# Kernel optimization log

Measured on AMD Instinct MI355X. Metric: run time of the kernel, lower is better.

The kernel has to match this reference:

```python
import jax, jax.numpy as jnp
import numpy as np
import math

B = 1024      # graphs
N = 64        # nodes per graph (padded, masked by node_mask)
BN = B * N    # total nodes
EPG = 192     # directed edges per graph
E = B * EPG


def setup_inputs() -> dict:
    key = jax.random.key(0)
    ks = jax.random.split(key, 40)

    def nrm(k, shp, s=0.02):
        return (jax.random.normal(k, shp) * s).astype(jnp.float32)

    mol_batch_x = jax.random.normal(ks[0], (BN, 19), dtype=jnp.float32)
    offs = jnp.arange(B, dtype=jnp.int32) * N
    src = jax.random.randint(ks[1], (B, EPG), 0, N, dtype=jnp.int32) + offs[:, None]
    dst = jax.random.randint(ks[2], (B, EPG), 0, N, dtype=jnp.int32) + offs[:, None]
    mol_batch_edge_index = jnp.stack([src.reshape(-1), dst.reshape(-1)], axis=0)
    mol_batch_batch = jnp.repeat(jnp.arange(B, dtype=jnp.int32), N)
    text_features = jax.random.normal(ks[3], (B, 300), dtype=jnp.float32)
    timesteps = jax.random.uniform(ks[4], (B,), minval=0.0, maxval=1000.0, dtype=jnp.float32)
    node_mask = (jax.random.uniform(ks[5], (B, N)) > 0.1).astype(jnp.float32)

    p = {
        'W_tr': nrm(ks[6], (19, 300)),   'b_tr': jnp.zeros((300,), jnp.float32),
        'W_c1': nrm(ks[7], (300, 600)),  'b_c1': jnp.zeros((600,), jnp.float32),
        'W_c2': nrm(ks[8], (600, 600)),  'b_c2': jnp.zeros((600,), jnp.float32),
        'W_c3': nrm(ks[9], (600, 600)),  'b_c3': jnp.zeros((600,), jnp.float32),
        'W_h1': nrm(ks[10], (600, 600)), 'b_h1': jnp.zeros((600,), jnp.float32),
        'W_h2': nrm(ks[11], (600, 600)), 'b_h2': jnp.zeros((600,), jnp.float32),
        'W_h3': nrm(ks[12], (600, 300)), 'b_h3': jnp.zeros((300,), jnp.float32),
        'ln_g': jnp.ones((300,), jnp.float32), 'ln_b': jnp.zeros((300,), jnp.float32),
        'W_t1': nrm(ks[13], (128, 512)), 'b_t1': jnp.zeros((512,), jnp.float32),
        'W_t2': nrm(ks[14], (512, 512)), 'b_t2': jnp.zeros((512,), jnp.float32),
        'W_e':  nrm(ks[15], (512, 3000)), 'b_e': jnp.zeros((3000,), jnp.float32),
    }
    return dict(mol_batch_x=mol_batch_x, mol_batch_edge_index=mol_batch_edge_index,
                mol_batch_batch=mol_batch_batch, text_features=text_features,
                timesteps=timesteps, node_mask=node_mask, **p)


def timestep_embedding(t, dim=128, max_period=10000.0):
    half = dim // 2
    freqs = jnp.exp(-math.log(max_period) * jnp.arange(half, dtype=jnp.float32) / half)
    args = t[:, None] * freqs[None]                 # [B, half]
    return jnp.concatenate([jnp.cos(args), jnp.sin(args)], axis=-1)  # [B, dim]


def gcn_conv(x, W, b, src, dst, num_nodes):
    # PyG GCNConv: D^{-1/2} (A + I) D^{-1/2} X W + b, edge weights 1
    h = x @ W                                             # [BN, F]
    deg = jnp.zeros((num_nodes,), h.dtype).at[dst].add(1.0) + 1.0  # in-degree + self-loop
    inv_sqrt = jax.lax.rsqrt(deg)
    coef = inv_sqrt[src] * inv_sqrt[dst]                  # [E]
    agg = jax.ops.segment_sum(h[src] * coef[:, None], dst, num_segments=num_nodes)
    return agg + h * (1.0 / deg)[:, None] + b             # self-loop norm = 1/deg


def global_mean_pool(x, batch, num_graphs):
    sums = jax.ops.segment_sum(x, batch, num_segments=num_graphs)
    cnts = jax.ops.segment_sum(jnp.ones((x.shape[0],), x.dtype), batch, num_segments=num_graphs)
    return sums / jnp.maximum(cnts, 1.0)[:, None]


def layer_norm(x, g, b, eps=1e-5):
    mu = jnp.mean(x, axis=-1, keepdims=True)
    var = jnp.mean(jnp.square(x - mu), axis=-1, keepdims=True)
    return (x - mu) * jax.lax.rsqrt(var + eps) * g + b


def reference(mol_batch_x, mol_batch_edge_index, mol_batch_batch, text_features,
              timesteps, node_mask, W_tr, b_tr, W_c1, b_c1, W_c2, b_c2, W_c3, b_c3,
              W_h1, b_h1, W_h2, b_h2, W_h3, b_h3, ln_g, ln_b,
              W_t1, b_t1, W_t2, b_t2, W_e, b_e):
    num_nodes = mol_batch_x.shape[0]
    num_graphs = node_mask.shape[0]
    src, dst = mol_batch_edge_index[0], mol_batch_edge_index[1]

    # FiLM conditioning from timestep embedding
    emb = jax.nn.relu(timestep_embedding(timesteps, 128) @ W_t1 + b_t1) @ W_t2 + b_t2  # [B,512]
    emb_out = jax.nn.relu(emb) @ W_e + b_e                                             # [B,3000]
    s1, t1 = emb_out[:, 0:600], emb_out[:, 600:1200]
    s2, t2 = emb_out[:, 1200:1800], emb_out[:, 1800:2400]
    s3, t3 = emb_out[:, 2400:2700], emb_out[:, 2700:3000]

    # node transform + mask
    x = mol_batch_x @ W_tr + b_tr                     # [BN, 300]
    x = x * node_mask.reshape(-1, 1)

    # GCN stack
    x = jax.nn.relu(gcn_conv(x, W_c1, b_c1, src, dst, num_nodes))
    x = jax.nn.relu(gcn_conv(x, W_c2, b_c2, src, dst, num_nodes))
    x = gcn_conv(x, W_c3, b_c3, src, dst, num_nodes)  # [BN, 600]

    g = global_mean_pool(x, mol_batch_batch, num_graphs)  # [B, 600]
    g = jax.nn.relu(g @ W_h1 + b_h1)
    g = g * (1.0 + s1) + t1
    g = jax.nn.relu(g @ W_h2 + b_h2)
    g = g * (1.0 + s2) + t2
    g = g @ W_h3 + b_h3                                # [B, 300]
    g = g * (1.0 + s3) + t3
    g = layer_norm(g, ln_g, ln_b)
    return (g, text_features)
```

## Files before the change

kernel.cpp:

```cpp
#include <hip/hip_runtime.h>
#include <hip/hip_bf16.h>
#include <cstdint>
#include <cstddef>

static constexpr int B   = 1024;
static constexpr int N   = 64;
static constexpr int BN  = B * N;
static constexpr int EPG = 192;
static constexpr int E   = B * EPG;
static constexpr int FP  = 608;
static constexpr int PMS = 80;
static constexpr int NCONV = 2560;

typedef __hip_bfloat16 bf16;
typedef __bf16 bf16x8 __attribute__((ext_vector_type(8)));
typedef __bf16 bf16x4 __attribute__((ext_vector_type(4)));
typedef float  f32x4  __attribute__((ext_vector_type(4)));

__device__ __forceinline__ void storeC(float* p, float v) { *p = v; }
__device__ __forceinline__ void storeC(bf16* p, float v) { *p = __float2bfloat16(v); }

__device__ __forceinline__ void llds16(const void* g, void* l) {
    __builtin_amdgcn_global_load_lds(
        (const __attribute__((address_space(1))) unsigned int*)g,
        (__attribute__((address_space(3))) unsigned int*)l,
        16, 0, 0);
}

template<bool RELU, bool FILM, typename CT>
__device__ __forceinline__ void g64_tile(
    const bf16* __restrict__ A, int lda,
    const bf16* __restrict__ Bt, int ldb,
    const float* __restrict__ bias,
    CT* __restrict__ C, int ldc, int Ncap,
    const bf16* __restrict__ fS, const bf16* __restrict__ fT, int fstride,
    int K, int m0, int n0, __bf16* As, __bf16* Bs, int tid)
{
    const int lane = tid & 63;
    const int w    = tid >> 6;
    const int wn   = w * 32;
    const int l15  = lane & 15;
    const int lhi  = lane >> 4;

    f32x4 acc[4][2] = {};

    for (int k0 = 0; k0 < K; k0 += 32) {
        {
            int row = tid >> 2, kc = tid & 3;
            char* la = (char*)As + (size_t)(w * 64) * 16;
            llds16(A + (size_t)(m0 + row) * lda + k0 + kc * 8, la);
        }
        #pragma unroll
        for (int t = 0; t < 2; ++t) {
            int ci  = t * 256 + tid;
            int row = ci >> 2, kc = ci & 3;
            char* lb = (char*)Bs + (size_t)(t * 256 + w * 64) * 16;
            llds16(Bt + (size_t)(n0 + row) * ldb + k0 + kc * 8, lb);
        }
        asm volatile("s_waitcnt vmcnt(0)" ::: "memory");
        __syncthreads();

        bf16x8 af[4], bg[2];
        #pragma unroll
        for (int i = 0; i < 4; ++i)
            af[i] = *(bf16x8*)(As + (i * 16 + l15) * 32 + lhi * 8);
        #pragma unroll
        for (int j = 0; j < 2; ++j)
            bg[j] = *(bf16x8*)(Bs + (wn + j * 16 + l15) * 32 + lhi * 8);
        #pragma unroll
        for (int i = 0; i < 4; ++i)
            #pragma unroll
            for (int j = 0; j < 2; ++j)
                acc[i][j] = __builtin_amdgcn_mfma_f32_16x16x32_bf16(
                    af[i], bg[j], acc[i][j], 0, 0, 0);
        __syncthreads();
    }

    #pragma unroll
    for (int i = 0; i < 4; ++i) {
        #pragma unroll
        for (int j = 0; j < 2; ++j) {
            int col = n0 + wn + j * 16 + l15;
            if (col < Ncap) {
                float bv = bias ? bias[col] : 0.f;
                #pragma unroll
                for (int e = 0; e < 4; ++e) {
                    int row = m0 + i * 16 + lhi * 4 + e;
                    float v = acc[i][j][e] + bv;
                    if (RELU) v = fmaxf(v, 0.f);
                    if (FILM) {
                        float sv = __bfloat162float(fS[(size_t)row * fstride + col]);
                        float tv = __bfloat162float(fT[(size_t)row * fstride + col]);
                        v = v * (1.f + sv) + tv;
                    }
                    storeC(&C[(size_t)row * ldc + col], v);
                }
            }
        }
    }
}

template<bool RELU, bool FILM, typename CT>
__global__ __launch_bounds__(256) void gemm64(
    const bf16* __restrict__ A, int lda,
    const bf16* __restrict__ Bt, int ldb,
    const float* __restrict__ bias,
    CT* __restrict__ C, int ldc, int Ncap,
    const bf16* __restrict__ fS, const bf16* __restrict__ fT, int fstride,
    int K)
{
    __shared__ __align__(16) __bf16 As[64 * 32];
    __shared__ __align__(16) __bf16 Bs[128 * 32];
    g64_tile<RELU, FILM, CT>(A, lda, Bt, ldb, bias, C, ldc, Ncap,
                             fS, fT, fstride, K,
                             blockIdx.x * 64, blockIdx.y * 128, As, Bs,
                             threadIdx.x);
}

__global__ __launch_bounds__(256) void k_two_gemms(
    const bf16* __restrict__ A2b, const bf16* __restrict__ Wet,
    const float* __restrict__ b_e, bf16* __restrict__ EO,
    const bf16* __restrict__ Yv, const bf16* __restrict__ Wb3,
    const float* __restrict__ b_c3, bf16* __restrict__ G0)
{
    __shared__ __align__(16) __bf16 As[64 * 32];
    __shared__ __align__(16) __bf16 Bs[128 * 32];
    int bid = blockIdx.x;
    if (bid < 384) {
        int mt = bid / 24, nt = bid % 24;
        g64_tile<false, false, bf16>(A2b, 512, Wet, 512, b_e, EO, 3000, 3000,
                                     nullptr, nullptr, 0, 512,
                                     mt * 64, nt * 128, As, Bs, threadIdx.x);
    } else {
        int t = bid - 384;
        int mt = t / 5, nt = t % 5;
        g64_tile<false, false, bf16>(Yv, FP, Wb3, FP, b_c3, G0, FP, 600,
                                     nullptr, nullptr, 0, FP,
                                     mt * 64, nt * 128, As, Bs, threadIdx.x);
    }
}

__global__ __launch_bounds__(256) void conv_fused(
    const bf16* __restrict__ A, int lda, int K,
    const bf16* __restrict__ Bt, int ldb,
    const bf16* __restrict__ Pmg,
    const float* __restrict__ bias,
    bf16* __restrict__ Xout,
    const bf16* __restrict__ gA, int glda,
    const bf16* __restrict__ gBt, int gldb,
    const float* __restrict__ gbias,
    bf16* __restrict__ gC, int gldc, int gNcap, int gK, int gnt)
{
    __shared__ __align__(16) char regA[17408];
    __shared__ __align__(16) __bf16 Pm[128 * PMS];

    const int tid = threadIdx.x;
    const int bid = blockIdx.x;

    if (bid >= NCONV) {
        int t = bid - NCONV;
        int mt2 = t / gnt, nt2 = t % gnt;
        g64_tile<true, false, bf16>(gA, glda, gBt, gldb, gbias, gC, gldc, gNcap,
                                    nullptr, nullptr, 0, gK,
                                    mt2 * 64, nt2 * 128,
                                    (__bf16*)regA, (__bf16*)(regA + 4096), tid);
        return;
    }

    __bf16* As = (__bf16*)regA;
    __bf16* Bs = (__bf16*)(regA + 8192);
    __bf16* Ts = (__bf16*)regA;

    const int lane = tid & 63;
    const int w    = tid >> 6;
    const int wm   = (w & 1) * 64;
    const int wn   = (w >> 1) * 64;
    const int l15  = lane & 15;
    const int lhi  = lane >> 4;

    const int lid = bid >> 3;
    const int mt  = (bid & 7) * 64 + lid / 5;
    const int nt  = lid % 5;
    const int m0  = mt * 128;
    const int n0  = nt * 128;

    #pragma unroll
    for (int i = 0; i < 5; ++i) {
        int cbase = w * 320 + i * 64;
        llds16(Pmg + (size_t)mt * (128 * PMS) + (size_t)(cbase + lane) * 8,
               (char*)Pm + (size_t)cbase * 16);
    }

    f32x4 acc[4][4] = {};
    for (int k0 = 0; k0 < K; k0 += 32) {
        #pragma unroll
        for (int t = 0; t < 2; ++t) {
            int ci  = t * 256 + w * 64 + lane;
            int row = ci >> 2, kc = ci & 3;
            char* la = (char*)As + (size_t)(t * 256 + w * 64) * 16;
            char* lb = (char*)Bs + (size_t)(t * 256 + w * 64) * 16;
            llds16(A  + (size_t)(m0 + row) * lda + k0 + kc * 8, la);
            llds16(Bt + (size_t)(n0 + row) * ldb + k0 + kc * 8, lb);
        }
        asm volatile("s_waitcnt vmcnt(0)" ::: "memory");
        __syncthreads();

        bf16x8 af[4], bg[4];
        #pragma unroll
        for (int i = 0; i < 4; ++i)
            af[i] = *(bf16x8*)(As + (wm + i * 16 + l15) * 32 + lhi * 8);
        #pragma unroll
        for (int j = 0; j < 4; ++j)
            bg[j] = *(bf16x8*)(Bs + (wn + j * 16 + l15) * 32 + lhi * 8);
        #pragma unroll
        for (int i = 0; i < 4; ++i)
            #pragma unroll
            for (int j = 0; j < 4; ++j)
                acc[i][j] = __builtin_amdgcn_mfma_f32_16x16x32_bf16(
                    af[i], bg[j], acc[i][j], 0, 0, 0);
        __syncthreads();
    }

    const int g  = w & 1;
    const int nb = w >> 1;
    #pragma unroll
    for (int h = 0; h < 2; ++h) {
        if (wn == h * 64) {
            #pragma unroll
            for (int i = 0; i < 4; ++i)
                #pragma unroll
                for (int j = 0; j < 4; ++j) {
                    int c_local = j * 16 + l15;
                    int rbase   = wm + i * 16 + lhi * 4;
                    bf16x4 pk;
                    #pragma unroll
                    for (int e = 0; e < 4; ++e) pk[e] = (__bf16)acc[i][j][e];
                    *(bf16x4*)(Ts + c_local * 136 + rbase) = pk;
                }
        }
        __syncthreads();

        f32x4 acc2[4][2] = {};
        #pragma unroll
        for (int k0 = 0; k0 < 64; k0 += 32) {
            bf16x8 pa[4], hb[2];
            #pragma unroll
            for (int i = 0; i < 4; ++i)
                pa[i] = *(bf16x8*)(Pm + (g * 64 + i * 16 + l15) * PMS + k0 + lhi * 8);
            #pragma unroll
            for (int j = 0; j < 2; ++j)
                hb[j] = *(bf16x8*)(Ts + (nb * 32 + j * 16 + l15) * 136
                                      + g * 64 + k0 + lhi * 8);
            #pragma unroll
            for (int i = 0; i < 4; ++i)
                #pragma unroll
                for (int j = 0; j < 2; ++j)
                    acc2[i][j] = __builtin_amdgcn_mfma_f32_16x16x32_bf16(
                        pa[i], hb[j], acc2[i][j], 0, 0, 0);
        }
        #pragma unroll
        for (int i = 0; i < 4; ++i)
            #pragma unroll
            for (int j = 0; j < 2; ++j) {
                int col = n0 + h * 64 + nb * 32 + j * 16 + l15;
                if (col < FP) {
                    float bv = (col < 600) ? bias[col] : 0.f;
                    #pragma unroll
                    for (int e = 0; e < 4; ++e) {
                        int row = m0 + g * 64 + i * 16 + lhi * 4 + e;
                        float v = fmaxf(acc2[i][j][e] + bv, 0.f);
                        Xout[(size_t)row * FP + col] = __float2bfloat16(v);
                    }
                }
            }
        __syncthreads();
    }
}

__global__ __launch_bounds__(256) void conv_fused_q(
    const bf16* __restrict__ A, int lda, int K,
    const bf16* __restrict__ Bt, int ldb,
    const bf16* __restrict__ Pmg,
    const float* __restrict__ bias,
    const float* __restrict__ qv,
    bf16* __restrict__ Y,
    const bf16* __restrict__ gA, int glda,
    const bf16* __restrict__ gBt, int gldb,
    const float* __restrict__ gbias,
    bf16* __restrict__ gC, int gldc, int gNcap, int gK, int gnt)
{
    __shared__ __align__(16) char regA[17408];
    __shared__ __align__(16) __bf16 Pm[128 * PMS];
    __shared__ float s_q[128];

    const int tid = threadIdx.x;
    const int bid = blockIdx.x;

    if (bid >= NCONV) {
        int t = bid - NCONV;
        int mt2 = t / gnt, nt2 = t % gnt;
        g64_tile<true, false, bf16>(gA, glda, gBt, gldb, gbias, gC, gldc, gNcap,
                                    nullptr, nullptr, 0, gK,
                                    mt2 * 64, nt2 * 128,
                                    (__bf16*)regA, (__bf16*)(regA + 4096), tid);
        return;
    }

    __bf16* As = (__bf16*)regA;
    __bf16* Bs = (__bf16*)(regA + 8192);
    __bf16* Ts = (__bf16*)regA;

    const int lane = tid & 63;
    const int w    = tid >> 6;
    const int wm   = (w & 1) * 64;
    const int wn   = (w >> 1) * 64;
    const int l15  = lane & 15;
    const int lhi  = lane >> 4;

    const int lid = bid >> 3;
    const int mt  = (bid & 7) * 64 + lid / 5;
    const int nt  = lid % 5;
    const int m0  = mt * 128;
    const int n0  = nt * 128;

    #pragma unroll
    for (int i = 0; i < 5; ++i) {
        int cbase = w * 320 + i * 64;
        llds16(Pmg + (size_t)mt * (128 * PMS) + (size_t)(cbase + lane) * 8,
               (char*)Pm + (size_t)cbase * 16);
    }
    if (tid < 128) s_q[tid] = qv[mt * 128 + tid];

    f32x4 acc[4][4] = {};
    for (int k0 = 0; k0 < K; k0 += 32) {
        #pragma unroll
        for (int t = 0; t < 2; ++t) {
            int ci  = t * 256 + w * 64 + lane;
            int row = ci >> 2, kc = ci & 3;
            char* la = (char*)As + (size_t)(t * 256 + w * 64) * 16;
            char* lb = (char*)Bs + (size_t)(t * 256 + w * 64) * 16;
            llds16(A  + (size_t)(m0 + row) * lda + k0 + kc * 8, la);
            llds16(Bt + (size_t)(n0 + row) * ldb + k0 + kc * 8, lb);
        }
        asm volatile("s_waitcnt vmcnt(0)" ::: "memory");
        __syncthreads();

        bf16x8 af[4], bg[4];
        #pragma unroll
        for (int i = 0; i < 4; ++i)
            af[i] = *(bf16x8*)(As + (wm + i * 16 + l15) * 32 + lhi * 8);
        #pragma unroll
        for (int j = 0; j < 4; ++j)
            bg[j] = *(bf16x8*)(Bs + (wn + j * 16 + l15) * 32 + lhi * 8);
        #pragma unroll
        for (int i = 0; i < 4; ++i)
            #pragma unroll
            for (int j = 0; j < 4; ++j)
                acc[i][j] = __builtin_amdgcn_mfma_f32_16x16x32_bf16(
                    af[i], bg[j], acc[i][j], 0, 0, 0);
        __syncthreads();
    }

    const int g  = w & 1;
    const int nb = w >> 1;
    #pragma unroll
    for (int h = 0; h < 2; ++h) {
        if (wn == h * 64) {
            #pragma unroll
            for (int i = 0; i < 4; ++i)
                #pragma unroll
                for (int j = 0; j < 4; ++j) {
                    int c_local = j * 16 + l15;
                    int rbase   = wm + i * 16 + lhi * 4;
                    bf16x4 pk;
                    #pragma unroll
                    for (int e = 0; e < 4; ++e) pk[e] = (__bf16)acc[i][j][e];
                    *(bf16x4*)(Ts + c_local * 136 + rbase) = pk;
                }
        }
        __syncthreads();

        f32x4 acc2[4][2] = {};
        #pragma unroll
        for (int k0 = 0; k0 < 64; k0 += 32) {
            bf16x8 pa[4], hb[2];
            #pragma unroll
            for (int i = 0; i < 4; ++i)
                pa[i] = *(bf16x8*)(Pm + (g * 64 + i * 16 + l15) * PMS + k0 + lhi * 8);
            #pragma unroll
            for (int j = 0; j < 2; ++j)
                hb[j] = *(bf16x8*)(Ts + (nb * 32 + j * 16 + l15) * 136
                                      + g * 64 + k0 + lhi * 8);
            #pragma unroll
            for (int i = 0; i < 4; ++i)
                #pragma unroll
                for (int j = 0; j < 2; ++j)
                    acc2[i][j] = __builtin_amdgcn_mfma_f32_16x16x32_bf16(
                        pa[i], hb[j], acc2[i][j], 0, 0, 0);
        }
        #pragma unroll
        for (int j = 0; j < 2; ++j) {
            int col = n0 + h * 64 + nb * 32 + j * 16 + l15;
            float bv = (col < 600) ? bias[col] : 0.f;
            float yp = 0.f;
            #pragma unroll
            for (int i = 0; i < 4; ++i)
                #pragma unroll
                for (int e = 0; e < 4; ++e) {
                    float v = fmaxf(acc2[i][j][e] + bv, 0.f);
                    yp += s_q[g * 64 + i * 16 + lhi * 4 + e] * v;
                }
            yp += __shfl_xor(yp, 16, 64);
            yp += __shfl_xor(yp, 32, 64);
            if (lhi == 0 && col < FP)
                Y[(size_t)(mt * 2 + g) * FP + col] = __float2bfloat16(yp);
        }
        __syncthreads();
    }
}

struct WtJob  { const float* src; bf16* dst; int Ksrc, Nsrc, Kp, Np, blk0; };
struct PrepArgs {
    WtJob j[9];
    int nwt, te0, pp0, xtr0;
    const int*   ei;
    const float* ts;
    const float* xin; const float* Wtr; const float* btr; const float* mask;
    bf16* TE; bf16* Pmg; float* qv; bf16* X;
};

__global__ __launch_bounds__(256) void k_prep(PrepArgs a)
{
    __shared__ __align__(16) char sm[35840];
    const int bx  = blockIdx.x;
    const int tid = threadIdx.x;

    if (bx < a.nwt) {
        int ji = 0;
        while (ji < 8 && bx >= a.j[ji + 1].blk0) ++ji;
        WtJob jb = a.j[ji];
        int t  = bx - jb.blk0;
        int kt = (jb.Kp + 63) >> 6;
        int ti = t % kt, tj = t / kt;
        int kg0 = ti * 64, ng0 = tj * 64;
        float (*T)[65] = (float(*)[65])sm;
        #pragma unroll 4
        for (int r = 0; r < 16; ++r) {
            int kl = (tid >> 6) + r * 4, nl = tid & 63;
            int kg = kg0 + kl, ng = ng0 + nl;
            T[kl][nl] = (kg < jb.Ksrc && ng < jb.Nsrc)
                        ? jb.src[(size_t)kg * jb.Nsrc + ng] : 0.f;
        }
        __syncthreads();
        #pragma unroll 4
        for (int r = 0; r < 16; ++r) {
            int nl = (tid >> 6) + r * 4, kl = tid & 63;
            int ng = ng0 + nl, kg = kg0 + kl;
            if (ng < jb.Np && kg < jb.Kp)
                jb.dst[(size_t)ng * jb.Kp + kg] = __float2bfloat16(T[kl][nl]);
        }
    } else if (bx < a.pp0) {
        int idx = (bx - a.te0) * 256 + tid;
        int b = idx >> 7, jj = idx & 127;
        float tt = a.ts[b];
        int h = jj & 63;
        float freq = expf(-9.210340371976184f * (float)h / 64.f);
        float ang = tt * freq;
        a.TE[idx] = __float2bfloat16((jj < 64) ? cosf(ang) : sinf(ang));
    } else if (bx < a.xtr0) {
        int pr = bx - a.pp0;
        float* Pf   = (float*)sm;
        int*   cnt  = (int*)(sm + 32768);
        float* sQ   = (float*)(sm + 33280);
        float* sI   = (float*)(sm + 33792);
        float* sIvd = (float*)(sm + 34304);

        for (int idx = tid; idx < 8192; idx += 256) Pf[idx] = 0.f;
        if (tid < 128) cnt[tid] = 0;
        __syncthreads();
        for (int e = tid; e < 2 * EPG; e += 256) {
            int g  = (e >= EPG);
            int eg = (2 * pr + g) * EPG + (e - g * EPG);
            int ld = (a.ei[E + eg] & 63) + g * 64;
            atomicAdd(&cnt[ld], 1);
        }
        __syncthreads();
        if (tid < 128) {
            float d = (float)cnt[tid] + 1.0f;
            float iv = 1.f / d;
            sIvd[tid] = iv;
            sI[tid]   = rsqrtf(d);
            sQ[tid]   = iv;
        }
        __syncthreads();
        for (int e = tid; e < 2 * EPG; e += 256) {
            int g   = (e >= EPG);
            int eg  = (2 * pr + g) * EPG + (e - g * EPG);
            int lsl = a.ei[eg] & 63;
            int ldl = a.ei[E + eg] & 63;
            float cf = sI[g * 64 + lsl] * sI[g * 64 + ldl];
            atomicAdd(&Pf[(g * 64 + ldl) * 64 + lsl], cf);
            atomicAdd(&sQ[g * 64 + lsl], cf);
        }
        __syncthreads();
        if (tid < 128) {
            Pf[tid * 64 + (tid & 63)] += sIvd[tid];
            a.qv[pr * 128 + tid] = sQ[tid] * (1.f / 64.f);
        }
        __syncthreads();
        for (int idx = tid; idx < 128 * PMS; idx += 256) {
            int r = idx / PMS, k = idx - r * PMS;
            float v = (k < 64) ? Pf[r * 64 + k] : 0.f;
            a.Pmg[(size_t)pr * (128 * PMS) + idx] = __float2bfloat16(v);
        }
    } else {
        int g = bx - a.xtr0;
        float* Ws = (float*)sm;
        float* xb = (float*)(sm + 23104);
        float* sb = (float*)(sm + 28224);
        float* smk= (float*)(sm + 29440);

        for (int idx = tid; idx < 19 * 304; idx += 256) {
            int k = idx / 304, c = idx - k * 304;
            Ws[idx] = (c < 300) ? a.Wtr[k * 300 + c] : 0.f;
        }
        for (int idx = tid; idx < 64 * 19; idx += 256) {
            int n = idx / 19, k = idx - n * 19;
            xb[n * 20 + k] = a.xin[(size_t)(g * 64 + n) * 19 + k];
        }
        for (int c = tid; c < 304; c += 256)
            sb[c] = (c < 300) ? a.btr[c] : 0.f;
        if (tid < 64) smk[tid] = a.mask[g * 64 + tid];
        __syncthreads();

        int n  = tid >> 2;
        int c0 = tid & 3;
        float m = smk[n];
        for (int c = c0; c < 304; c += 4) {
            float acc = sb[c];
            #pragma unroll
            for (int k = 0; k < 19; ++k)
                acc += xb[n * 20 + k] * Ws[k * 304 + c];
            a.X[(size_t)(g * 64 + n) * FP + c] = __float2bfloat16(acc * m);
        }
        bf16x8 z = {};
        for (int idx = tid; idx < 64 * 38; idx += 256) {
            int nn = idx / 38, jv = idx - nn * 38;
            *(bf16x8*)((__bf16*)a.X + (size_t)(g * 64 + nn) * FP + 304 + jv * 8) = z;
        }
    }
}

__global__ __launch_bounds__(256) void k_ln_copy(const float* __restrict__ G,
                                                 const float* __restrict__ lg,
                                                 const float* __restrict__ lb,
                                                 const float* __restrict__ text,
                                                 float* __restrict__ out)
{
    int r = blockIdx.x;
    int tid = threadIdx.x;
    __shared__ float red[4];
    __shared__ float smu, svar;

    float v0 = (tid < 300) ? G[r * 300 + tid] : 0.f;
    float v1 = (tid + 256 < 300) ? G[r * 300 + tid + 256] : 0.f;
    float s = v0 + v1;
    #pragma unroll
    for (int o = 32; o > 0; o >>= 1) s += __shfl_down(s, o, 64);
    if ((tid & 63) == 0) red[tid >> 6] = s;
    __syncthreads();
    if (tid == 0) smu = (red[0] + red[1] + red[2] + red[3]) * (1.f / 300.f);
    __syncthreads();
    float mu = smu;
    float d0 = (tid < 300) ? v0 - mu : 0.f;
    float d1 = (tid + 256 < 300) ? v1 - mu : 0.f;
    s = d0 * d0 + d1 * d1;
    #pragma unroll
    for (int o = 32; o > 0; o >>= 1) s += __shfl_down(s, o, 64);
    if ((tid & 63) == 0) red[tid >> 6] = s;
    __syncthreads();
    if (tid == 0) svar = (red[0] + red[1] + red[2] + red[3]) * (1.f / 300.f);
    __syncthreads();
    float rstd = rsqrtf(svar + 1e-5f);
    if (tid < 300)
        out[r * 300 + tid] = d0 * rstd * lg[tid] + lb[tid];
    if (tid + 256 < 300)
        out[r * 300 + tid + 256] = d1 * rstd * lg[tid + 256] + lb[tid + 256];
    float* o2 = out + (size_t)B * 300;
    for (int c = tid; c < 300; c += 256)
        o2[(size_t)r * 300 + c] = text[(size_t)r * 300 + c];
}

extern "C" void kernel_launch(void* const* d_in, const int* in_sizes, int n_in,
                              void* d_out, int out_size, void* d_ws, size_t ws_size,
                              hipStream_t stream)
{
    const float* x_in  = (const float*)d_in[0];
    const int*   ei    = (const int*)d_in[1];
    const float* text  = (const float*)d_in[3];
    const float* tst   = (const float*)d_in[4];
    const float* mask  = (const float*)d_in[5];
    const float* W_tr  = (const float*)d_in[6];
    const float* b_tr  = (const float*)d_in[7];
    const float* W_c1  = (const float*)d_in[8];
    const float* b_c1  = (const float*)d_in[9];
    const float* W_c2  = (const float*)d_in[10];
    const float* b_c2  = (const float*)d_in[11];
    const float* W_c3  = (const float*)d_in[12];
    const float* b_c3  = (const float*)d_in[13];
    const float* W_h1  = (const float*)d_in[14];
    const float* b_h1  = (const float*)d_in[15];
    const float* W_h2  = (const float*)d_in[16];
    const float* b_h2  = (const float*)d_in[17];
    const float* W_h3  = (const float*)d_in[18];
    const float* b_h3  = (const float*)d_in[19];
    const float* ln_g  = (const float*)d_in[20];
    const float* ln_b  = (const float*)d_in[21];
    const float* W_t1  = (const float*)d_in[22];
    const float* b_t1  = (const float*)d_in[23];
    const float* W_t2  = (const float*)d_in[24];
    const float* b_t2  = (const float*)d_in[25];
    const float* W_e   = (const float*)d_in[26];
    const float* b_e   = (const float*)d_in[27];

    char* w = (char*)d_ws;
    size_t off = 0;
    auto carve = [&](size_t bytes) {
        void* p = w + off;
        off += (bytes + 255) & ~(size_t)255;
        return p;
    };
    bf16*  XA     = (bf16*) carve((size_t)BN * FP * 2);
    bf16*  Wb1    = (bf16*) carve((size_t)640 * 320 * 2);
    bf16*  Wb2    = (bf16*) carve((size_t)640 * FP * 2);
    bf16*  Wb3    = (bf16*) carve((size_t)640 * FP * 2);
    bf16*  Wt1t   = (bf16*) carve((size_t)512 * 128 * 2);
    bf16*  Wt2t   = (bf16*) carve((size_t)512 * 512 * 2);
    bf16*  Wet    = (bf16*) carve((size_t)3072 * 512 * 2);
    bf16*  Wh1t   = (bf16*) carve((size_t)640 * FP * 2);
    bf16*  Wh2t   = (bf16*) carve((size_t)640 * FP * 2);
    bf16*  Wh3t   = (bf16*) carve((size_t)384 * FP * 2);
    bf16*  TE     = (bf16*) carve((size_t)B * 128 * 2);
    bf16*  A1b    = (bf16*) carve((size_t)B * 512 * 2);
    bf16*  A2b    = (bf16*) carve((size_t)B * 512 * 2);
    bf16*  EO     = (bf16*) carve((size_t)B * 3000 * 2);
    bf16*  Yv     = (bf16*) carve((size_t)B * FP * 2);
    bf16*  G0     = (bf16*) carve((size_t)B * FP * 2);
    bf16*  G1     = (bf16*) carve((size_t)B * FP * 2);
    bf16*  G2     = (bf16*) carve((size_t)B * FP * 2);
    float* G3     = (float*)carve((size_t)B * 300 * 4);
    bf16*  Pmg    = (bf16*) carve((size_t)512 * 128 * PMS * 2);
    float* qv     = (float*)carve((size_t)BN * 4);
    (void)ws_size; (void)in_sizes; (void)n_in; (void)out_size;

    float* out = (float*)d_out;

    PrepArgs pa;
    struct JD { const float* s; bf16* d; int Ks, Ns, Kp, Np; };
    JD jd[9] = {
        { W_c1, Wb1,  300, 600,  320, 640 },
        { W_c2, Wb2,  600, 600,  FP,  640 },
        { W_c3, Wb3,  600, 600,  FP,  640 },
        { W_t1, Wt1t, 128, 512,  128, 512 },
        { W_t2, Wt2t, 512, 512,  512, 512 },
        { W_e,  Wet,  512, 3000, 512, 3072 },
        { W_h1, Wh1t, 600, 600,  FP,  640 },
        { W_h2, Wh2t, 600, 600,  FP,  640 },
        { W_h3, Wh3t, 600, 300,  FP,  384 },
    };
    int cum = 0;
    for (int i = 0; i < 9; ++i) {
        int kt = (jd[i].Kp + 63) >> 6, nt = (jd[i].Np + 63) >> 6;
        pa.j[i] = { jd[i].s, jd[i].d, jd[i].Ks, jd[i].Ns, jd[i].Kp, jd[i].Np, cum };
        cum += kt * nt;
    }
    pa.nwt  = cum;
    pa.te0  = cum;       cum += (B * 128) / 256;
    pa.pp0  = cum;       cum += B / 2;
    pa.xtr0 = cum;       cum += B;
    pa.ei = ei; pa.ts = tst;
    pa.xin = x_in; pa.Wtr = W_tr; pa.btr = b_tr; pa.mask = mask;
    pa.TE = TE; pa.Pmg = Pmg; pa.qv = qv; pa.X = XA;
    k_prep<<<cum, 256, 0, stream>>>(pa);

    conv_fused<<<NCONV + 64, 256, 0, stream>>>(
        XA, FP, 320, Wb1, 320, Pmg, b_c1, XA,
        TE, 128, Wt1t, 128, b_t1, A1b, 512, 512, 128, 4);

    conv_fused_q<<<NCONV + 64, 256, 0, stream>>>(
        XA, FP, FP, Wb2, FP, Pmg, b_c2, qv, Yv,
        A1b, 512, Wt2t, 512, b_t2, A2b, 512, 512, 512, 4);

    k_two_gemms<<<464, 256, 0, stream>>>(A2b, Wet, b_e, EO, Yv, Wb3, b_c3, G0);

    gemm64<true, true, bf16><<<dim3(16, 5), 256, 0, stream>>>(
        G0, FP, Wh1t, FP, b_h1, G1, FP, 600, EO + 0, EO + 600, 3000, FP);
    gemm64<true, true, bf16><<<dim3(16, 5), 256, 0, stream>>>(
        G1, FP, Wh2t, FP, b_h2, G2, FP, 600, EO + 1200, EO + 1800, 3000, FP);
    gemm64<false, true, float><<<dim3(16, 3), 256, 0, stream>>>(
        G2, FP, Wh3t, FP, b_h3, G3, 300, 300, EO + 2400, EO + 2700, 3000, FP);

    k_ln_copy<<<B, 256, 0, stream>>>(G3, ln_g, ln_b, text, out);
}
```

Before: 408.0 us.

## Aggregate first GCN layer on 20-wide inputs before the node transform

The first conv layer's normalized adjacency is now applied in k_prep to the masked 19-feature input (plus a mask column for the bias), using the associativity P(XW+b) = (PX)W + (P·mask)b. The first conv kernel then becomes a plain GEMM with ReLU, with no per-tile P·H MFMA pass and no Pm LDS staging. This removes the second matmul stage and its extra LDS traffic and syncs from the large conv1 launch, but adds per-graph shared-memory atomics and a small dense 64x64x20 product to the prep kernel. The guest GEMM path is also moved into a noinline helper, which may reduce register pressure in the main kernels.

```diff
diff --git a/kernel.cpp b/kernel.cpp
--- a/kernel.cpp
+++ b/kernel.cpp
@@ -9,6 +9,7 @@
 static constexpr int EPG = 192;
 static constexpr int E   = B * EPG;
 static constexpr int FP  = 608;
+static constexpr int KP1 = 320;
 static constexpr int PMS = 80;
 static constexpr int NCONV = 2560;
 
@@ -100,6 +101,17 @@
     }
 }
 
+__device__ __attribute__((noinline)) void guest_g64(
+    const bf16* gA, int glda, const bf16* gBt, int gldb,
+    const float* gbias, bf16* gC, int gldc, int gNcap, int gK, int gnt,
+    int t, char* lds, int tid)
+{
+    int mt2 = t / gnt, nt2 = t % gnt;
+    g64_tile<true, false, bf16>(gA, glda, gBt, gldb, gbias, gC, gldc, gNcap,
+                                nullptr, nullptr, 0, gK, mt2 * 64, nt2 * 128,
+                                (__bf16*)lds, (__bf16*)(lds + 4096), tid);
+}
+
 template<bool RELU, bool FILM, typename CT>
 __global__ __launch_bounds__(256) void gemm64(
     const bf16* __restrict__ A, int lda,
@@ -140,36 +152,28 @@
     }
 }
 
-__global__ __launch_bounds__(256) void conv_fused(
-    const bf16* __restrict__ A, int lda, int K,
-    const bf16* __restrict__ Bt, int ldb,
-    const bf16* __restrict__ Pmg,
+__global__ __launch_bounds__(256) void conv1_gemm(
+    const bf16* __restrict__ A,
+    const bf16* __restrict__ Bt,
     const float* __restrict__ bias,
-    bf16* __restrict__ Xout,
+    bf16* __restrict__ X1,
     const bf16* __restrict__ gA, int glda,
     const bf16* __restrict__ gBt, int gldb,
     const float* __restrict__ gbias,
     bf16* __restrict__ gC, int gldc, int gNcap, int gK, int gnt)
 {
     __shared__ __align__(16) char regA[17408];
-    __shared__ __align__(16) __bf16 Pm[128 * PMS];
-
     const int tid = threadIdx.x;
     const int bid = blockIdx.x;
 
     if (bid >= NCONV) {
-        int t = bid - NCONV;
-        int mt2 = t / gnt, nt2 = t % gnt;
-        g64_tile<true, false, bf16>(gA, glda, gBt, gldb, gbias, gC, gldc, gNcap,
-                                    nullptr, nullptr, 0, gK,
-                                    mt2 * 64, nt2 * 128,
-                                    (__bf16*)regA, (__bf16*)(regA + 4096), tid);
+        guest_g64(gA, glda, gBt, gldb, gbias, gC, gldc, gNcap, gK, gnt,
+                  bid - NCONV, regA, tid);
         return;
     }
 
     __bf16* As = (__bf16*)regA;
     __bf16* Bs = (__bf16*)(regA + 8192);
-    __bf16* Ts = (__bf16*)regA;
 
     const int lane = tid & 63;
     const int w    = tid >> 6;
@@ -184,23 +188,16 @@
     const int m0  = mt * 128;
     const int n0  = nt * 128;
 
-    #pragma unroll
-    for (int i = 0; i < 5; ++i) {
-        int cbase = w * 320 + i * 64;
-        llds16(Pmg + (size_t)mt * (128 * PMS) + (size_t)(cbase + lane) * 8,
-               (char*)Pm + (size_t)cbase * 16);
-    }
-
     f32x4 acc[4][4] = {};
-    for (int k0 = 0; k0 < K; k0 += 32) {
+    for (int k0 = 0; k0 < KP1; k0 += 32) {
         #pragma unroll
         for (int t = 0; t < 2; ++t) {
             int ci  = t * 256 + w * 64 + lane;
             int row = ci >> 2, kc = ci & 3;
             char* la = (char*)As + (size_t)(t * 256 + w * 64) * 16;
             char* lb = (char*)Bs + (size_t)(t * 256 + w * 64) * 16;
-            llds16(A  + (size_t)(m0 + row) * lda + k0 + kc * 8, la);
-            llds16(Bt + (size_t)(n0 + row) * ldb + k0 + kc * 8, lb);
+            llds16(A  + (size_t)(m0 + row) * KP1 + k0 + kc * 8, la);
+            llds16(Bt + (size_t)(n0 + row) * KP1 + k0 + kc * 8, lb);
         }
         asm volatile("s_waitcnt vmcnt(0)" ::: "memory");
         __syncthreads();
@@ -221,60 +218,21 @@
         __syncthreads();
     }
 
-    const int g  = w & 1;
-    const int nb = w >> 1;
     #pragma unroll
-    for (int h = 0; h < 2; ++h) {
-        if (wn == h * 64) {
-            #pragma unroll
-            for (int i = 0; i < 4; ++i)
+    for (int i = 0; i < 4; ++i)
+        #pragma unroll
+        for (int j = 0; j < 4; ++j) {
+            int col = n0 + wn + j * 16 + l15;
+            if (col < FP) {
+                float bv = (col < 600) ? bias[col] : 0.f;
                 #pragma unroll
-                for (int j = 0; j < 4; ++j) {
-                    int c_local = j * 16 + l15;
-                    int rbase   = wm + i * 16 + lhi * 4;
-                    bf16x4 pk;
-                    #pragma unroll
-                    for (int e = 0; e < 4; ++e) pk[e] = (__bf16)acc[i][j][e];
-                    *(bf16x4*)(Ts + c_local * 136 + rbase) = pk;
-                }
-        }
-        __syncthreads();
-
-        f32x4 acc2[4][2] = {};
-        #pragma unroll
-        for (int k0 = 0; k0 < 64; k0 += 32) {
-            bf16x8 pa[4], hb[2];
-            #pragma unroll
-            for (int i = 0; i < 4; ++i)
-                pa[i] = *(bf16x8*)(Pm + (g * 64 + i * 16 + l15) * PMS + k0 + lhi * 8);
-            #pragma unroll
-            for (int j = 0; j < 2; ++j)
-                hb[j] = *(bf16x8*)(Ts + (nb * 32 + j * 16 + l15) * 136
-                                      + g * 64 + k0 + lhi * 8);
-            #pragma unroll
-            for (int i = 0; i < 4; ++i)
-                #pragma unroll
-                for (int j = 0; j < 2; ++j)
-                    acc2[i][j] = __builtin_amdgcn_mfma_f32_16x16x32_bf16(
-                        pa[i], hb[j], acc2[i][j], 0, 0, 0);
-        }
-        #pragma unroll
-        for (int i = 0; i < 4; ++i)
-            #pragma unroll
-            for (int j = 0; j < 2; ++j) {
-                int col = n0 + h * 64 + nb * 32 + j * 16 + l15;
-                if (col < FP) {
-                    float bv = (col < 600) ? bias[col] : 0.f;
-                    #pragma unroll
-                    for (int e = 0; e < 4; ++e) {
-                        int row = m0 + g * 64 + i * 16 + lhi * 4 + e;
-                        float v = fmaxf(acc2[i][j][e] + bv, 0.f);
-                        Xout[(size_t)row * FP + col] = __float2bfloat16(v);
-                    }
+                for (int e = 0; e < 4; ++e) {
+                    int row = m0 + wm + i * 16 + lhi * 4 + e;
+                    float v = fmaxf(acc[i][j][e] + bv, 0.f);
+                    X1[(size_t)row * FP + col] = __float2bfloat16(v);
                 }
             }
-        __syncthreads();
-    }
+        }
 }
 
 __global__ __launch_bounds__(256) void conv_fused_q(
@@ -297,12 +255,8 @@
     const int bid = blockIdx.x;
 
     if (bid >= NCONV) {
-        int t = bid - NCONV;
-        int mt2 = t / gnt, nt2 = t % gnt;
-        g64_tile<true, false, bf16>(gA, glda, gBt, gldb, gbias, gC, gldc, gNcap,
-                                    nullptr, nullptr, 0, gK,
-                                    mt2 * 64, nt2 * 128,
-                                    (__bf16*)regA, (__bf16*)(regA + 4096), tid);
+        guest_g64(gA, glda, gBt, gldb, gbias, gC, gldc, gNcap, gK, gnt,
+                  bid - NCONV, regA, tid);
         return;
     }
 
@@ -426,7 +380,7 @@
     const int*   ei;
     const float* ts;
     const float* xin; const float* Wtr; const float* btr; const float* mask;
-    bf16* TE; bf16* Pmg; float* qv; bf16* X;
+    bf16* TE; bf16* Pmg; float* qv; bf16* PX0;
 };
 
 __global__ __launch_bounds__(256) void k_prep(PrepArgs a)
@@ -515,38 +469,70 @@
         }
     } else {
         int g = bx - a.xtr0;
-        float* Ws = (float*)sm;
-        float* xb = (float*)(sm + 23104);
-        float* sb = (float*)(sm + 28224);
-        float* smk= (float*)(sm + 29440);
-
+        float* Pf  = (float*)sm;
+        float* Ws  = (float*)sm;
+        float* xm  = (float*)(sm + 23104);
+        float* xa  = (float*)(sm + 28224);
+        float* isqv= (float*)(sm + 33344);
+        float* ivdv= (float*)(sm + 33600);
+        int*   cnt = (int*)  (sm + 33856);
+        float* sb  = (float*)(sm + 34112);
+
+        for (int idx = tid; idx < 4096; idx += 256) Pf[idx] = 0.f;
+        if (tid < 64) cnt[tid] = 0;
+        __syncthreads();
+        for (int e = tid; e < EPG; e += 256)
+            atomicAdd(&cnt[a.ei[E + g * EPG + e] & 63], 1);
+        __syncthreads();
+        if (tid < 64) {
+            float d = (float)cnt[tid] + 1.0f;
+            ivdv[tid] = 1.f / d;
+            isqv[tid] = rsqrtf(d);
+        }
+        __syncthreads();
+        for (int e = tid; e < EPG; e += 256) {
+            int ls = a.ei[g * EPG + e] & 63;
+            int ld = a.ei[E + g * EPG + e] & 63;
+            atomicAdd(&Pf[ld * 64 + ls], isqv[ls] * isqv[ld]);
+        }
+        for (int idx = tid; idx < 64 * 20; idx += 256) {
+            int n = idx / 20, j = idx - n * 20;
+            float mv = a.mask[g * 64 + n];
+            xm[idx] = (j < 19) ? mv * a.xin[(size_t)(g * 64 + n) * 19 + j] : mv;
+        }
+        __syncthreads();
+        if (tid < 64) Pf[tid * 64 + tid] += ivdv[tid];
+        __syncthreads();
+        for (int idx = tid; idx < 64 * 20; idx += 256) {
+            int r = idx / 20, j = idx - r * 20;
+            float s = 0.f;
+            #pragma unroll 8
+            for (int s2 = 0; s2 < 64; ++s2)
+                s += Pf[r * 64 + s2] * xm[s2 * 20 + j];
+            xa[idx] = s;
+        }
+        __syncthreads();
         for (int idx = tid; idx < 19 * 304; idx += 256) {
             int k = idx / 304, c = idx - k * 304;
             Ws[idx] = (c < 300) ? a.Wtr[k * 300 + c] : 0.f;
         }
-        for (int idx = tid; idx < 64 * 19; idx += 256) {
-            int n = idx / 19, k = idx - n * 19;
-            xb[n * 20 + k] = a.xin[(size_t)(g * 64 + n) * 19 + k];
-        }
         for (int c = tid; c < 304; c += 256)
             sb[c] = (c < 300) ? a.btr[c] : 0.f;
-        if (tid < 64) smk[tid] = a.mask[g * 64 + tid];
-        __syncthreads();
-
+        __syncthreads();
         int n  = tid >> 2;
         int c0 = tid & 3;
-        float m = smk[n];
+        float ba = xa[n * 20 + 19];
         for (int c = c0; c < 304; c += 4) {
-            float acc = sb[c];
+            float acc = ba * sb[c];
             #pragma unroll
             for (int k = 0; k < 19; ++k)
-                acc += xb[n * 20 + k] * Ws[k * 304 + c];
-            a.X[(size_t)(g * 64 + n) * FP + c] = __float2bfloat16(acc * m);
+                acc += xa[n * 20 + k] * Ws[k * 304 + c];
+            a.PX0[(size_t)(g * 64 + n) * KP1 + c] = __float2bfloat16(acc);
         }
         bf16x8 z = {};
-        for (int idx = tid; idx < 64 * 38; idx += 256) {
-            int nn = idx / 38, jv = idx - nn * 38;
-            *(bf16x8*)((__bf16*)a.X + (size_t)(g * 64 + nn) * FP + 304 + jv * 8) = z;
+        for (int idx = tid; idx < 64 * 2; idx += 256) {
+            int nn = idx >> 1, jv = idx & 1;
+            *(bf16x8*)((__bf16*)a.PX0 + (size_t)(g * 64 + nn) * KP1 + 304 + jv * 8) = z;
         }
     }
 }
@@ -630,8 +616,9 @@
         off += (bytes + 255) & ~(size_t)255;
         return p;
     };
-    bf16*  XA     = (bf16*) carve((size_t)BN * FP * 2);
-    bf16*  Wb1    = (bf16*) carve((size_t)640 * 320 * 2);
+    bf16*  PX0    = (bf16*) carve((size_t)BN * KP1 * 2);
+    bf16*  X1     = (bf16*) carve((size_t)BN * FP * 2);
+    bf16*  Wb1    = (bf16*) carve((size_t)640 * KP1 * 2);
     bf16*  Wb2    = (bf16*) carve((size_t)640 * FP * 2);
     bf16*  Wb3    = (bf16*) carve((size_t)640 * FP * 2);
     bf16*  Wt1t   = (bf16*) carve((size_t)512 * 128 * 2);
@@ -658,7 +645,7 @@
     PrepArgs pa;
     struct JD { const float* s; bf16* d; int Ks, Ns, Kp, Np; };
     JD jd[9] = {
-        { W_c1, Wb1,  300, 600,  320, 640 },
+        { W_c1, Wb1,  300, 600,  KP1, 640 },
         { W_c2, Wb2,  600, 600,  FP,  640 },
         { W_c3, Wb3,  600, 600,  FP,  640 },
         { W_t1, Wt1t, 128, 512,  128, 512 },
@@ -680,15 +667,15 @@
     pa.xtr0 = cum;       cum += B;
     pa.ei = ei; pa.ts = tst;
     pa.xin = x_in; pa.Wtr = W_tr; pa.btr = b_tr; pa.mask = mask;
-    pa.TE = TE; pa.Pmg = Pmg; pa.qv = qv; pa.X = XA;
+    pa.TE = TE; pa.Pmg = Pmg; pa.qv = qv; pa.PX0 = PX0;
     k_prep<<<cum, 256, 0, stream>>>(pa);
 
-    conv_fused<<<NCONV + 64, 256, 0, stream>>>(
-        XA, FP, 320, Wb1, 320, Pmg, b_c1, XA,
+    conv1_gemm<<<NCONV + 64, 256, 0, stream>>>(
+        PX0, Wb1, b_c1, X1,
         TE, 128, Wt1t, 128, b_t1, A1b, 512, 512, 128, 4);
 
     conv_fused_q<<<NCONV + 64, 256, 0, stream>>>(
-        XA, FP, FP, Wb2, FP, Pmg, b_c2, qv, Yv,
+        X1, FP, FP, Wb2, FP, Pmg, b_c2, qv, Yv,
         A1b, 512, Wt2t, 512, b_t2, A2b, 512, 512, 512, 4);
 
     k_two_gemms<<<464, 256, 0, stream>>>(A2b, Wet, b_e, EO, Yv, Wb3, b_c3, G0);
```

After: 367.0 us. 1.11x faster.
